# Optimization experiments

Hardware: AMD Instinct MI355X
Metric: run time of the kernel (lower is better)

The kernel has to match this reference:

```python
import jax, jax.numpy as jnp
import numpy as np


def setup_inputs() -> dict:
    key = jax.random.key(0)
    k1, k2, k3, k4 = jax.random.split(key, 4)
    B, S, E, A = 4, 4096, 1024, 1024
    embedded = jax.random.normal(k1, (B, S, E), dtype=jnp.float32)
    # nn.Linear(E, A, bias=False) weights, stored as [E, A] so y = x @ W
    Wk = jax.random.normal(k2, (E, A), dtype=jnp.float32) * (E ** -0.5)
    Wq = jax.random.normal(k3, (E, A), dtype=jnp.float32) * (E ** -0.5)
    Wv = jax.random.normal(k4, (E, A), dtype=jnp.float32) * (E ** -0.5)
    return {"embedded": embedded, "Wk": Wk, "Wq": Wq, "Wv": Wv}


def reference(embedded, Wk, Wq, Wv):
    # K, Q, V projections: [B, S, A]
    K = embedded @ Wk
    Q = embedded @ Wq
    V = embedded @ Wv
    A = K.shape[-1]
    S = embedded.shape[1]
    # causal scores [B, S, S]
    scores = jnp.einsum("bqa,bka->bqk", Q, K) / jnp.sqrt(jnp.float32(A))
    causal = jnp.tril(jnp.ones((S, S), dtype=bool))
    scores = jnp.where(causal, scores, -jnp.inf)
    probs = jax.nn.softmax(scores, axis=-1)
    out = jnp.einsum("bqk,bka->bqa", probs, V)
    # torch.round(out, decimals=4)
    return jnp.round(out, 4)
```

## Files before the change

kernel.cpp:

```cpp
#include <hip/hip_runtime.h>
#include <hip/hip_fp16.h>

typedef __attribute__((ext_vector_type(4))) float f32x4;
typedef __attribute__((ext_vector_type(8))) short s16x8;
typedef __attribute__((ext_vector_type(4))) short s16x4;
typedef unsigned short u16;
typedef unsigned int u32;

__device__ __forceinline__ u16 f2bf(float f) {
    union { float f; unsigned u; } x; x.f = f;
    return (u16)((x.u + 0x7fffu + ((x.u >> 16) & 1u)) >> 16);
}

__device__ __forceinline__ void ld16(const void* g, void* l) {
    __builtin_amdgcn_global_load_lds(
        (const __attribute__((address_space(1))) unsigned int*)g,
        (__attribute__((address_space(3))) unsigned int*)l, 16, 0, 0);
}

__device__ __forceinline__ void kstep(const u16* gA0, const u16* gA1,
                                      const u16* gB0, const u16* gB1,
                                      u16* sA, u16* sB,
                                      u16* dA0, u16* dA1, u16* dB0, u16* dB1,
                                      int wm, int wn, int lm, int lg, int sx,
                                      f32x4 acc[4][4])
{
    __syncthreads();
    ld16(gA0, dA0);
    ld16(gA1, dA1);
    ld16(gB0, dB0);
    ld16(gB1, dB1);
    __syncthreads();

    s16x8 af[4], bf[4];
    const int co = (lg ^ sx) * 8;
#pragma unroll
    for (int i = 0; i < 4; i++) {
        af[i] = *(const s16x8*)&sA[(wm + i * 16 + lm) * 32 + co];
        bf[i] = *(const s16x8*)&sB[(wn + i * 16 + lm) * 32 + co];
    }
#pragma unroll
    for (int i = 0; i < 4; i++)
#pragma unroll
        for (int j = 0; j < 4; j++)
            acc[i][j] = __builtin_amdgcn_mfma_f32_16x16x32_bf16(af[i], bf[j], acc[i][j], 0, 0, 0);
}

__device__ __forceinline__ void gemm_core(const u16* A, long lda, const u16* B, long ldb,
                                          int m0, int n0, int kEnd,
                                          f32x4 acc[4][4], u16* sA, u16* sB)
{
    const int t    = threadIdx.x;
    const int lane = t & 63;
    const int wave = t >> 6;
    const int wm   = (wave & 1) << 6;
    const int wn   = (wave >> 1) << 6;
    const int lm   = lane & 15;
    const int lg   = lane >> 4;
    const int sx   = (lm >> 1) & 3;
    const int sr   = t >> 2;
    const int sc   = (((t & 3) ^ ((t >> 3) & 3)) << 3);
    const u16* gA0 = A + (long)(m0 + sr) * lda + sc;
    const u16* gA1 = A + (long)(m0 + 64 + sr) * lda + sc;
    const u16* gB0 = B + (long)(n0 + sr) * ldb + sc;
    const u16* gB1 = B + (long)(n0 + 64 + sr) * ldb + sc;
    u16* dA0 = sA + t * 8;  u16* dA1 = sA + 2048 + t * 8;
    u16* dB0 = sB + t * 8;  u16* dB1 = sB + 2048 + t * 8;

    for (int k0 = 0; k0 < kEnd; k0 += 32)
        kstep(gA0 + k0, gA1 + k0, gB0 + k0, gB1 + k0,
              sA, sB, dA0, dA1, dB0, dB1, wm, wn, lm, lg, sx, acc);
}

__global__ void convert_x(const float* __restrict__ X, u16* __restrict__ Xb) {
    long idx = ((long)blockIdx.x * 256 + threadIdx.x) * 4;
    f32x4 v = *(const f32x4*)&X[idx];
    s16x4 o;
    o.x = (short)f2bf(v.x); o.y = (short)f2bf(v.y);
    o.z = (short)f2bf(v.z); o.w = (short)f2bf(v.w);
    *(s16x4*)&Xb[idx] = o;
}

__global__ void convert_w(const float* __restrict__ Wk, const float* __restrict__ Wq,
                          const float* __restrict__ Wv,
                          u16* __restrict__ Wkt, u16* __restrict__ Wqt, u16* __restrict__ Wvt) {
    const float* W; u16* O;
    if (blockIdx.y == 0)      { W = Wk; O = Wkt; }
    else if (blockIdx.y == 1) { W = Wq; O = Wqt; }
    else                      { W = Wv; O = Wvt; }
    __shared__ u16 tile[64][65];
    int k0 = (blockIdx.x >> 4) << 6, n0 = (blockIdx.x & 15) << 6;
    int t = threadIdx.x;
    int rr = t >> 4, cc = (t & 15) << 2;
#pragma unroll
    for (int i = 0; i < 4; i++) {
        int row = rr + i * 16;
        f32x4 v = *(const f32x4*)&W[(long)(k0 + row) * 1024 + n0 + cc];
        tile[row][cc + 0] = f2bf(v.x); tile[row][cc + 1] = f2bf(v.y);
        tile[row][cc + 2] = f2bf(v.z); tile[row][cc + 3] = f2bf(v.w);
    }
    __syncthreads();
#pragma unroll
    for (int i = 0; i < 4; i++) {
        int row = rr + i * 16;
        s16x4 pk;
        pk.x = (short)tile[cc + 0][row]; pk.y = (short)tile[cc + 1][row];
        pk.z = (short)tile[cc + 2][row]; pk.w = (short)tile[cc + 3][row];
        *(s16x4*)&O[(long)(n0 + row) * 1024 + k0 + cc] = pk;
    }
}

__global__ __launch_bounds__(256, 2) void proj_all(const u16* __restrict__ X,
                                                   const u16* __restrict__ Wqt,
                                                   const u16* __restrict__ Wkt,
                                                   const u16* __restrict__ Wvt,
                                                   u16* __restrict__ Qb,
                                                   u16* __restrict__ Kb,
                                                   u16* __restrict__ Vt) {
    __shared__ u16 sA[4096], sB[4096];
    int z = blockIdx.x >> 10;
    int q = blockIdx.x & 1023;
    int m0 = (q >> 3) * 128, n0 = (q & 7) * 128;
    const u16* Wt = (z == 0) ? Wqt : (z == 1) ? Wkt : Wvt;
    f32x4 acc[4][4] = {};
    gemm_core(X, 1024, Wt, 1024, m0, n0, 1024, acc, sA, sB);

    int lane = threadIdx.x & 63, wave = threadIdx.x >> 6;
    int wm = (wave & 1) << 6, wn = (wave >> 1) << 6, lm = lane & 15, lg = lane >> 4;
    if (z < 2) {
        u16* O = (z == 0) ? Qb : Kb;
#pragma unroll
        for (int i = 0; i < 4; i++)
#pragma unroll
            for (int j = 0; j < 4; j++)
#pragma unroll
                for (int r = 0; r < 4; r++) {
                    int row = m0 + wm + i * 16 + lg * 4 + r;
                    int col = n0 + wn + j * 16 + lm;
                    O[(long)row * 1024 + col] = f2bf(acc[i][j][r]);
                }
    } else {
#pragma unroll
        for (int i = 0; i < 4; i++)
#pragma unroll
            for (int j = 0; j < 4; j++) {
                int row0 = m0 + wm + i * 16 + lg * 4;
                int col  = n0 + wn + j * 16 + lm;
                int b = row0 >> 12, s = row0 & 4095;
                s16x4 pk;
                pk.x = (short)f2bf(acc[i][j][0]); pk.y = (short)f2bf(acc[i][j][1]);
                pk.z = (short)f2bf(acc[i][j][2]); pk.w = (short)f2bf(acc[i][j][3]);
                *(s16x4*)&Vt[(long)b * 4194304 + (long)col * 4096 + s] = pk;
            }
    }
}

__global__ __launch_bounds__(256, 2) void sgemm_causal(const u16* __restrict__ Q,
                                                       const u16* __restrict__ K,
                                                       u16* __restrict__ S) {
    __shared__ u16 sA[4096], sB[4096];
    int b  = blockIdx.x / 528;
    int tt = blockIdx.x % 528;
    int it = (int)((sqrtf(8.0f * tt + 1.0f) - 1.0f) * 0.5f);
    while ((it + 1) * (it + 2) / 2 <= tt) ++it;
    while (it * (it + 1) / 2 > tt) --it;
    int jt = tt - it * (it + 1) / 2;

    const u16* A  = Q + (long)b * 4194304;
    const u16* Bt = K + (long)b * 4194304;
    f32x4 acc[4][4] = {};
    gemm_core(A, 1024, Bt, 1024, it * 128, jt * 128, 1024, acc, sA, sB);

    u16* Sp = S + (long)(b * 528 + tt) * 16384;
    int lane = threadIdx.x & 63, wave = threadIdx.x >> 6;
    int wm = (wave & 1) << 6, wn = (wave >> 1) << 6, lm = lane & 15, lg = lane >> 4;
#pragma unroll
    for (int i = 0; i < 4; i++)
#pragma unroll
        for (int j = 0; j < 4; j++)
#pragma unroll
            for (int r = 0; r < 4; r++) {
                int ri = wm + i * 16 + lg * 4 + r;
                int cj = wn + j * 16 + lm;
                float v = acc[i][j][r] * 0.03125f;
                if (jt * 128 + cj > it * 128 + ri) v = -30000.0f;
                Sp[ri * 128 + cj] = __half_as_ushort(__float2half(v));
            }
}

__global__ __launch_bounds__(256) void row_softmax(u16* __restrict__ S,
                                                   float* __restrict__ inv_l) {
    int wave = threadIdx.x >> 6, lane = threadIdx.x & 63;
    int gr = blockIdx.x * 4 + wave;
    int b  = gr >> 12;
    int r  = gr & 4095;
    int it = r >> 7, ri = r & 127;
    u16* base = S + (long)(b * 528 + it * (it + 1) / 2) * 16384 + ri * 128;
    int c = lane * 2;

    float m = -1e30f;
    for (int jt = 0; jt <= it; jt++) {
        u32 v = *(const u32*)&base[jt * 16384 + c];
        float a0 = __half2float(__ushort_as_half((u16)(v & 0xffff)));
        float a1 = __half2float(__ushort_as_half((u16)(v >> 16)));
        m = fmaxf(m, fmaxf(a0, a1));
    }
#pragma unroll
    for (int o = 32; o; o >>= 1) m = fmaxf(m, __shfl_xor(m, o, 64));

    const float LOG2E = 1.44269504088896f;
    float l = 0.0f;
    for (int jt = 0; jt <= it; jt++) {
        u32 v = *(const u32*)&base[jt * 16384 + c];
        float a0 = __half2float(__ushort_as_half((u16)(v & 0xffff)));
        float a1 = __half2float(__ushort_as_half((u16)(v >> 16)));
        float p0 = exp2f((a0 - m) * LOG2E);
        float p1 = exp2f((a1 - m) * LOG2E);
        u32 o = (u32)f2bf(p0) | ((u32)f2bf(p1) << 16);
        *(u32*)&base[jt * 16384 + c] = o;
        l += p0 + p1;
    }
#pragma unroll
    for (int o = 32; o; o >>= 1) l += __shfl_xor(l, o, 64);
    if (lane == 0) inv_l[gr] = 1.0f / l;
}

__global__ __launch_bounds__(256, 2) void pv_gemm(const u16* __restrict__ P,
                                                  const u16* __restrict__ Vt,
                                                  const float* __restrict__ inv_l,
                                                  float* __restrict__ Out) {
    __shared__ u16 sA[4096], sB[4096];
    int g   = blockIdx.x;
    int it  = 31 - (g >> 5);
    int rem = g & 31;
    int b   = rem >> 3;
    int at  = rem & 7;

    const int t    = threadIdx.x;
    const int lane = t & 63;
    const int wave = t >> 6;
    const int wm   = (wave & 1) << 6;
    const int wn   = (wave >> 1) << 6;
    const int lm   = lane & 15;
    const int lg   = lane >> 4;
    const int sx   = (lm >> 1) & 3;
    const int sr   = t >> 2;
    const int sc   = (((t & 3) ^ ((t >> 3) & 3)) << 3);

    const u16* Pbase = P + (long)(b * 528 + it * (it + 1) / 2) * 16384;
    const u16* gA0 = Pbase + sr * 128 + sc;
    const u16* gA1 = gA0 + 64 * 128;
    const u16* gB0 = Vt + (long)b * 4194304 + (long)(at * 128 + sr) * 4096 + sc;
    const u16* gB1 = gB0 + (long)64 * 4096;
    u16* dA0 = sA + t * 8;  u16* dA1 = sA + 2048 + t * 8;
    u16* dB0 = sB + t * 8;  u16* dB1 = sB + 2048 + t * 8;

    f32x4 acc[4][4] = {};
    for (int jt = 0; jt <= it; jt++) {
        long aoff = (long)jt * 16384;
        long boff = (long)jt * 128;
#pragma unroll
        for (int kk = 0; kk < 128; kk += 32)
            kstep(gA0 + aoff + kk, gA1 + aoff + kk, gB0 + boff + kk, gB1 + boff + kk,
                  sA, sB, dA0, dA1, dB0, dB1, wm, wn, lm, lg, sx, acc);
    }

#pragma unroll
    for (int i = 0; i < 4; i++)
#pragma unroll
        for (int j = 0; j < 4; j++)
#pragma unroll
            for (int r = 0; r < 4; r++) {
                int gi = it * 128 + wm + i * 16 + lg * 4 + r;
                int ga = at * 128 + wn + j * 16 + lm;
                Out[((long)b * 4096 + gi) * 1024 + ga] = acc[i][j][r] * inv_l[b * 4096 + gi];
            }
}

extern "C" void kernel_launch(void* const* d_in, const int* in_sizes, int n_in,
                              void* d_out, int out_size, void* d_ws, size_t ws_size,
                              hipStream_t stream) {
    const float* X  = (const float*)d_in[0];
    const float* Wk = (const float*)d_in[1];
    const float* Wq = (const float*)d_in[2];
    const float* Wv = (const float*)d_in[3];
    float* Out = (float*)d_out;

    char* w = (char*)d_ws;
    u16*   Qb   = (u16*)(w);
    u16*   Kb   = (u16*)(w + 33554432);
    u16*   Vt   = (u16*)(w + 67108864);
    float* invl = (float*)(w + 100663296);
    u16*   Xb   = (u16*)(w + 100728832);
    u16*   Wqt  = (u16*)(w + 134283264);
    u16*   Wkt  = (u16*)(w + 136380416);
    u16*   Wvt  = (u16*)(w + 138477568);
    u16*   S    = (u16*)(w + 100728832);

    convert_x<<<16384, 256, 0, stream>>>(X, Xb);
    convert_w<<<dim3(256, 3), 256, 0, stream>>>(Wk, Wq, Wv, Wkt, Wqt, Wvt);
    proj_all<<<3072, 256, 0, stream>>>(Xb, Wqt, Wkt, Wvt, Qb, Kb, Vt);
    sgemm_causal<<<4 * 528, 256, 0, stream>>>(Qb, Kb, S);
    row_softmax<<<4096, 256, 0, stream>>>(S, invl);
    pv_gemm<<<1024, 256, 0, stream>>>(S, Vt, invl, Out);
}
```

Before: 509.8 us.

## Widen GEMM tiles to 128x256 so each A tile feeds two B tiles

All three GEMM kernels (projection, causal score, PV) now compute two adjacent 128-wide output tiles per block. They share one A tile in LDS and keep two accumulator sets, which halves A-tile global loads and LDS traffic per MFMA and halves the grid size. The causal score kernel pairs column tiles within each triangular row and skips the store for the second tile when it falls past the diagonal, which means some wasted compute on diagonal rows. Register pressure doubles (32 f32x4 accumulators), and fewer blocks may reduce occupancy and load balance.

```diff
diff --git a/kernel.cpp b/kernel.cpp
--- a/kernel.cpp
+++ b/kernel.cpp
@@ -18,37 +18,46 @@
         (__attribute__((address_space(3))) unsigned int*)l, 16, 0, 0);
 }
 
-__device__ __forceinline__ void kstep(const u16* gA0, const u16* gA1,
-                                      const u16* gB0, const u16* gB1,
-                                      u16* sA, u16* sB,
-                                      u16* dA0, u16* dA1, u16* dB0, u16* dB1,
-                                      int wm, int wn, int lm, int lg, int sx,
-                                      f32x4 acc[4][4])
+__device__ __forceinline__ void kstep2(const u16* gA0, const u16* gA1,
+                                       const u16* gB0, const u16* gB1,
+                                       const u16* gC0, const u16* gC1,
+                                       u16* sA, u16* sB,
+                                       int wm, int wn, int lm, int lg, int sx,
+                                       f32x4 acc0[4][4], f32x4 acc1[4][4])
 {
+    const int t = threadIdx.x;
+    u16* dA0 = sA + t * 8;        u16* dA1 = sA + 2048 + t * 8;
+    u16* dB0 = sB + t * 8;        u16* dB1 = sB + 2048 + t * 8;
+    u16* dC0 = sB + 4096 + t * 8; u16* dC1 = sB + 6144 + t * 8;
+
     __syncthreads();
-    ld16(gA0, dA0);
-    ld16(gA1, dA1);
-    ld16(gB0, dB0);
-    ld16(gB1, dB1);
+    ld16(gA0, dA0); ld16(gA1, dA1);
+    ld16(gB0, dB0); ld16(gB1, dB1);
+    ld16(gC0, dC0); ld16(gC1, dC1);
     __syncthreads();
 
-    s16x8 af[4], bf[4];
+    s16x8 af[4], bf[4], cf[4];
     const int co = (lg ^ sx) * 8;
 #pragma unroll
     for (int i = 0; i < 4; i++) {
         af[i] = *(const s16x8*)&sA[(wm + i * 16 + lm) * 32 + co];
         bf[i] = *(const s16x8*)&sB[(wn + i * 16 + lm) * 32 + co];
+        cf[i] = *(const s16x8*)&sB[4096 + (wn + i * 16 + lm) * 32 + co];
     }
 #pragma unroll
     for (int i = 0; i < 4; i++)
 #pragma unroll
-        for (int j = 0; j < 4; j++)
-            acc[i][j] = __builtin_amdgcn_mfma_f32_16x16x32_bf16(af[i], bf[j], acc[i][j], 0, 0, 0);
-}
-
-__device__ __forceinline__ void gemm_core(const u16* A, long lda, const u16* B, long ldb,
-                                          int m0, int n0, int kEnd,
-                                          f32x4 acc[4][4], u16* sA, u16* sB)
+        for (int j = 0; j < 4; j++) {
+            acc0[i][j] = __builtin_amdgcn_mfma_f32_16x16x32_bf16(af[i], bf[j], acc0[i][j], 0, 0, 0);
+            acc1[i][j] = __builtin_amdgcn_mfma_f32_16x16x32_bf16(af[i], cf[j], acc1[i][j], 0, 0, 0);
+        }
+}
+
+__device__ __forceinline__ void gemm_core2(const u16* A, long lda,
+                                           const u16* B0, const u16* B1, long ldb,
+                                           int m0, int kEnd,
+                                           f32x4 acc0[4][4], f32x4 acc1[4][4],
+                                           u16* sA, u16* sB)
 {
     const int t    = threadIdx.x;
     const int lane = t & 63;
@@ -62,14 +71,14 @@
     const int sc   = (((t & 3) ^ ((t >> 3) & 3)) << 3);
     const u16* gA0 = A + (long)(m0 + sr) * lda + sc;
     const u16* gA1 = A + (long)(m0 + 64 + sr) * lda + sc;
-    const u16* gB0 = B + (long)(n0 + sr) * ldb + sc;
-    const u16* gB1 = B + (long)(n0 + 64 + sr) * ldb + sc;
-    u16* dA0 = sA + t * 8;  u16* dA1 = sA + 2048 + t * 8;
-    u16* dB0 = sB + t * 8;  u16* dB1 = sB + 2048 + t * 8;
+    const u16* gB0 = B0 + (long)sr * ldb + sc;
+    const u16* gB1 = B0 + (long)(64 + sr) * ldb + sc;
+    const u16* gC0 = B1 + (long)sr * ldb + sc;
+    const u16* gC1 = B1 + (long)(64 + sr) * ldb + sc;
 
     for (int k0 = 0; k0 < kEnd; k0 += 32)
-        kstep(gA0 + k0, gA1 + k0, gB0 + k0, gB1 + k0,
-              sA, sB, dA0, dA1, dB0, dB1, wm, wn, lm, lg, sx, acc);
+        kstep2(gA0 + k0, gA1 + k0, gB0 + k0, gB1 + k0, gC0 + k0, gC1 + k0,
+               sA, sB, wm, wn, lm, lg, sx, acc0, acc1);
 }
 
 __global__ void convert_x(const float* __restrict__ X, u16* __restrict__ Xb) {
@@ -117,13 +126,16 @@
                                                    u16* __restrict__ Qb,
                                                    u16* __restrict__ Kb,
                                                    u16* __restrict__ Vt) {
-    __shared__ u16 sA[4096], sB[4096];
-    int z = blockIdx.x >> 10;
-    int q = blockIdx.x & 1023;
-    int m0 = (q >> 3) * 128, n0 = (q & 7) * 128;
+    __shared__ u16 sA[4096], sB[8192];
+    int z   = blockIdx.x >> 9;
+    int rem = blockIdx.x & 511;
+    int m0  = (rem >> 2) * 128;
+    int n0  = (rem & 3) * 256;
     const u16* Wt = (z == 0) ? Wqt : (z == 1) ? Wkt : Wvt;
-    f32x4 acc[4][4] = {};
-    gemm_core(X, 1024, Wt, 1024, m0, n0, 1024, acc, sA, sB);
+
+    f32x4 acc0[4][4] = {}, acc1[4][4] = {};
+    gemm_core2(X, 1024, Wt + (long)n0 * 1024, Wt + (long)(n0 + 128) * 1024, 1024,
+               m0, 1024, acc0, acc1, sA, sB);
 
     int lane = threadIdx.x & 63, wave = threadIdx.x >> 6;
     int wm = (wave & 1) << 6, wn = (wave >> 1) << 6, lm = lane & 15, lg = lane >> 4;
@@ -137,7 +149,8 @@
                 for (int r = 0; r < 4; r++) {
                     int row = m0 + wm + i * 16 + lg * 4 + r;
                     int col = n0 + wn + j * 16 + lm;
-                    O[(long)row * 1024 + col] = f2bf(acc[i][j][r]);
+                    O[(long)row * 1024 + col]       = f2bf(acc0[i][j][r]);
+                    O[(long)row * 1024 + col + 128] = f2bf(acc1[i][j][r]);
                 }
     } else {
 #pragma unroll
@@ -147,10 +160,13 @@
                 int row0 = m0 + wm + i * 16 + lg * 4;
                 int col  = n0 + wn + j * 16 + lm;
                 int b = row0 >> 12, s = row0 & 4095;
-                s16x4 pk;
-                pk.x = (short)f2bf(acc[i][j][0]); pk.y = (short)f2bf(acc[i][j][1]);
-                pk.z = (short)f2bf(acc[i][j][2]); pk.w = (short)f2bf(acc[i][j][3]);
-                *(s16x4*)&Vt[(long)b * 4194304 + (long)col * 4096 + s] = pk;
+                s16x4 p0, p1;
+                p0.x = (short)f2bf(acc0[i][j][0]); p0.y = (short)f2bf(acc0[i][j][1]);
+                p0.z = (short)f2bf(acc0[i][j][2]); p0.w = (short)f2bf(acc0[i][j][3]);
+                p1.x = (short)f2bf(acc1[i][j][0]); p1.y = (short)f2bf(acc1[i][j][1]);
+                p1.z = (short)f2bf(acc1[i][j][2]); p1.w = (short)f2bf(acc1[i][j][3]);
+                *(s16x4*)&Vt[(long)b * 4194304 + (long)col * 4096 + s]         = p0;
+                *(s16x4*)&Vt[(long)b * 4194304 + (long)(col + 128) * 4096 + s] = p1;
             }
     }
 }
@@ -158,20 +174,27 @@
 __global__ __launch_bounds__(256, 2) void sgemm_causal(const u16* __restrict__ Q,
                                                        const u16* __restrict__ K,
                                                        u16* __restrict__ S) {
-    __shared__ u16 sA[4096], sB[4096];
-    int b  = blockIdx.x / 528;
-    int tt = blockIdx.x % 528;
-    int it = (int)((sqrtf(8.0f * tt + 1.0f) - 1.0f) * 0.5f);
-    while ((it + 1) * (it + 2) / 2 <= tt) ++it;
-    while (it * (it + 1) / 2 > tt) --it;
-    int jt = tt - it * (it + 1) / 2;
+    __shared__ u16 sA[4096], sB[8192];
+    int b  = blockIdx.x / 272;
+    int tt = blockIdx.x % 272;
+    int it = (int)(2.0f * sqrtf((float)tt + 1.0f)) - 1;
+    if (it > 31) it = 31;
+    if (it < 0) it = 0;
+    while (it < 31 && (((it + 2) * (it + 2)) >> 2) <= tt) ++it;
+    while (it > 0 && (((it + 1) * (it + 1)) >> 2) > tt) --it;
+    int jp  = tt - (((it + 1) * (it + 1)) >> 2);
+    int jt0 = jp * 2, jt1 = jt0 + 1;
+    bool valid1 = (jt1 <= it);
 
     const u16* A  = Q + (long)b * 4194304;
-    const u16* Bt = K + (long)b * 4194304;
-    f32x4 acc[4][4] = {};
-    gemm_core(A, 1024, Bt, 1024, it * 128, jt * 128, 1024, acc, sA, sB);
-
-    u16* Sp = S + (long)(b * 528 + tt) * 16384;
+    const u16* Kb = K + (long)b * 4194304;
+    f32x4 acc0[4][4] = {}, acc1[4][4] = {};
+    gemm_core2(A, 1024, Kb + (long)jt0 * 131072, Kb + (long)jt1 * 131072, 1024,
+               it * 128, 1024, acc0, acc1, sA, sB);
+
+    long tribase = (long)(b * 528 + ((it * (it + 1)) >> 1));
+    u16* Sp0 = S + (tribase + jt0) * 16384;
+    u16* Sp1 = S + (tribase + jt1) * 16384;
     int lane = threadIdx.x & 63, wave = threadIdx.x >> 6;
     int wm = (wave & 1) << 6, wn = (wave >> 1) << 6, lm = lane & 15, lg = lane >> 4;
 #pragma unroll
@@ -182,9 +205,15 @@
             for (int r = 0; r < 4; r++) {
                 int ri = wm + i * 16 + lg * 4 + r;
                 int cj = wn + j * 16 + lm;
-                float v = acc[i][j][r] * 0.03125f;
-                if (jt * 128 + cj > it * 128 + ri) v = -30000.0f;
-                Sp[ri * 128 + cj] = __half_as_ushort(__float2half(v));
+                int gi = it * 128 + ri;
+                float v0 = acc0[i][j][r] * 0.03125f;
+                if (jt0 * 128 + cj > gi) v0 = -30000.0f;
+                Sp0[ri * 128 + cj] = __half_as_ushort(__float2half(v0));
+                if (valid1) {
+                    float v1 = acc1[i][j][r] * 0.03125f;
+                    if (jt1 * 128 + cj > gi) v1 = -30000.0f;
+                    Sp1[ri * 128 + cj] = __half_as_ushort(__float2half(v1));
+                }
             }
 }
 
@@ -195,7 +224,7 @@
     int b  = gr >> 12;
     int r  = gr & 4095;
     int it = r >> 7, ri = r & 127;
-    u16* base = S + (long)(b * 528 + it * (it + 1) / 2) * 16384 + ri * 128;
+    u16* base = S + (long)(b * 528 + ((it * (it + 1)) >> 1)) * 16384 + ri * 128;
     int c = lane * 2;
 
     float m = -1e30f;
@@ -229,12 +258,12 @@
                                                   const u16* __restrict__ Vt,
                                                   const float* __restrict__ inv_l,
                                                   float* __restrict__ Out) {
-    __shared__ u16 sA[4096], sB[4096];
-    int g   = blockIdx.x;
-    int it  = 31 - (g >> 5);
-    int rem = g & 31;
-    int b   = rem >> 3;
-    int at  = rem & 7;
+    __shared__ u16 sA[4096], sB[8192];
+    int g  = blockIdx.x;
+    int it = (g < 256) ? (31 - (g >> 4)) : ((g - 256) >> 4);
+    int rem = g & 15;
+    int b   = rem >> 2;
+    int atp = rem & 3;
 
     const int t    = threadIdx.x;
     const int lane = t & 63;
@@ -247,22 +276,24 @@
     const int sr   = t >> 2;
     const int sc   = (((t & 3) ^ ((t >> 3) & 3)) << 3);
 
-    const u16* Pbase = P + (long)(b * 528 + it * (it + 1) / 2) * 16384;
+    const u16* Pbase = P + (long)(b * 528 + ((it * (it + 1)) >> 1)) * 16384;
     const u16* gA0 = Pbase + sr * 128 + sc;
     const u16* gA1 = gA0 + 64 * 128;
-    const u16* gB0 = Vt + (long)b * 4194304 + (long)(at * 128 + sr) * 4096 + sc;
+    const u16* gB0 = Vt + (long)b * 4194304 + (long)(atp * 256 + sr) * 4096 + sc;
     const u16* gB1 = gB0 + (long)64 * 4096;
-    u16* dA0 = sA + t * 8;  u16* dA1 = sA + 2048 + t * 8;
-    u16* dB0 = sB + t * 8;  u16* dB1 = sB + 2048 + t * 8;
-
-    f32x4 acc[4][4] = {};
+    const u16* gC0 = gB0 + (long)128 * 4096;
+    const u16* gC1 = gB0 + (long)192 * 4096;
+
+    f32x4 acc0[4][4] = {}, acc1[4][4] = {};
     for (int jt = 0; jt <= it; jt++) {
         long aoff = (long)jt * 16384;
         long boff = (long)jt * 128;
 #pragma unroll
         for (int kk = 0; kk < 128; kk += 32)
-            kstep(gA0 + aoff + kk, gA1 + aoff + kk, gB0 + boff + kk, gB1 + boff + kk,
-                  sA, sB, dA0, dA1, dB0, dB1, wm, wn, lm, lg, sx, acc);
+            kstep2(gA0 + aoff + kk, gA1 + aoff + kk,
+                   gB0 + boff + kk, gB1 + boff + kk,
+                   gC0 + boff + kk, gC1 + boff + kk,
+                   sA, sB, wm, wn, lm, lg, sx, acc0, acc1);
     }
 
 #pragma unroll
@@ -272,8 +303,10 @@
 #pragma unroll
             for (int r = 0; r < 4; r++) {
                 int gi = it * 128 + wm + i * 16 + lg * 4 + r;
-                int ga = at * 128 + wn + j * 16 + lm;
-                Out[((long)b * 4096 + gi) * 1024 + ga] = acc[i][j][r] * inv_l[b * 4096 + gi];
+                int ga = atp * 256 + wn + j * 16 + lm;
+                float s = inv_l[b * 4096 + gi];
+                Out[((long)b * 4096 + gi) * 1024 + ga]       = acc0[i][j][r] * s;
+                Out[((long)b * 4096 + gi) * 1024 + ga + 128] = acc1[i][j][r] * s;
             }
 }
 
@@ -299,8 +332,8 @@
 
     convert_x<<<16384, 256, 0, stream>>>(X, Xb);
     convert_w<<<dim3(256, 3), 256, 0, stream>>>(Wk, Wq, Wv, Wkt, Wqt, Wvt);
-    proj_all<<<3072, 256, 0, stream>>>(Xb, Wqt, Wkt, Wvt, Qb, Kb, Vt);
-    sgemm_causal<<<4 * 528, 256, 0, stream>>>(Qb, Kb, S);
+    proj_all<<<1536, 256, 0, stream>>>(Xb, Wqt, Wkt, Wvt, Qb, Kb, Vt);
+    sgemm_causal<<<1088, 256, 0, stream>>>(Qb, Kb, S);
     row_softmax<<<4096, 256, 0, stream>>>(S, invl);
-    pv_gemm<<<1024, 256, 0, stream>>>(S, Vt, invl, Out);
-}
+    pv_gemm<<<512, 256, 0, stream>>>(S, Vt, invl, Out);
+}
```

New measurement: 496.5 us. 2.6% less time.
